# Kernel tuning notes

Measured on AMD Instinct MI355X. Metric: run time of the kernel, lower is better.

Reference implementation:

```python
import jax, jax.numpy as jnp
import numpy as np

B, S, D, V, K, H, L, U = 256, 50, 32, 10000, 16, 64, 2, 32
NORM = 0.01


def setup_inputs() -> dict:
    key = jax.random.key(0)
    ks = iter(jax.random.split(key, 64))
    r = lambda *sh: jax.random.normal(next(ks), sh, dtype=jnp.float32) * 0.05
    inp = {
        'x1': r(B, U), 'z1': r(B, S, D), 'x2': r(B, U), 'z2': r(B, S, D),
        'embd': r(V, D),
        'dec_w1': r(D, H), 'dec_b1': r(H), 'dec_w2': r(H, D), 'dec_b2': r(D),
        'i_wih': r(3 * D, D), 'i_whh': r(3 * D, D), 'i_bih': r(3 * D), 'i_bhh': r(3 * D),
        'c_wih': r(3 * D, D), 'c_whh': r(3 * D, D), 'c_bih': r(3 * D), 'c_bhh': r(3 * D),
        'im_w1': r(D, D), 'im_b1': r(D), 'im_w2': r(D, D), 'im_b2': r(D),
        'cm_w1': r(D, D), 'cm_b1': r(D), 'cm_w2': r(D, D), 'cm_b2': r(D),
        'hw1': r(L, D, K * K), 'hb1': r(L, K * K), 'hw2': r(L, D, K * K), 'hb2': r(L, K * K),
        'lin_w': r(L, U, K), 'lin_b': r(L, K), 'lout_w': r(L, K, U), 'lout_b': r(L, U),
        'sample_num': B, 'trigger_seq_length': 30,
    }
    return inp


def _gru(x, wih, whh, bih, bhh):
    # PyTorch GRU, batch_first, h0 = 0; gate order (r, z, n)
    gi = jnp.einsum('bsd,ed->bse', x, wih) + bih  # [B,S,3D]

    def step(h, gi_t):
        gh = h @ whh.T + bhh
        gir, giz, gin = jnp.split(gi_t, 3, axis=-1)
        ghr, ghz, ghn = jnp.split(gh, 3, axis=-1)
        rr = jax.nn.sigmoid(gir + ghr)
        zz = jax.nn.sigmoid(giz + ghz)
        nn = jnp.tanh(gin + rr * ghn)
        h = (1.0 - zz) * nn + zz * h
        return h, h

    h0 = jnp.zeros((x.shape[0], whh.shape[1]), x.dtype)
    _, hs = jax.lax.scan(step, h0, jnp.swapaxes(gi, 0, 1))
    return jnp.swapaxes(hs, 0, 1)  # [B,S,D]


def _forward(x1, z1, x2, z2, embd, dec_w1, dec_b1, dec_w2, dec_b2,
             i_wih, i_whh, i_bih, i_bhh, c_wih, c_whh, c_bih, c_bhh,
             im_w1, im_b1, im_w2, im_b2, cm_w1, cm_b1, cm_w2, cm_b2,
             hw1, hb1, hw2, hb2, lin_w, lin_b, lout_w, lout_b,
             sample_num, trigger_seq_length):
    # --- VQVAE.find_nearest: cdist + argmin + gather (index path has no grad) ---
    q = jax.lax.stop_gradient(z1)
    t = jax.lax.stop_gradient(embd)
    # ||q - t||^2 expanded; argmin over sqrt == argmin over squared dist
    d2 = ((q * q).sum(-1)[:, :, None]
          - 2.0 * jnp.einsum('bsd,vd->bsv', q, t)
          + (t * t).sum(-1)[None, None, :])  # [B,S,V]
    idx = jnp.argmin(d2, axis=2)  # [B,S]
    z_emb = embd[idx]  # [B,S,D], gradient flows into embd via gather

    # --- VQVAE.decode ---
    h = jax.nn.leaky_relu(z_emb @ dec_w1 + dec_b1, negative_slope=0.1)
    z_recon = h @ dec_w2 + dec_b2  # [B,S,D]

    total_loss = jnp.mean((z2 - jax.lax.stop_gradient(z_emb)) ** 2)

    # --- item branch: GRU -> pick trigger step -> MLP (tanh, linear) ---
    hs = _gru(z_recon, i_wih, i_whh, i_bih, i_bhh)
    u1 = hs[:, trigger_seq_length, :]
    z1f = jnp.tanh(u1 @ im_w1 + im_b1) @ im_w2 + im_b2  # [B,D]

    # --- category branch ---
    hs = _gru(z2, c_wih, c_whh, c_bih, c_bhh)
    u2 = hs[:, trigger_seq_length, :]
    z2f = jnp.tanh(u2 @ cm_w1 + cm_b1) @ cm_w2 + cm_b2  # [B,D]

    # --- hypernetwork layers (activations in self.modules are never applied) ---
    out = x1
    for i in range(L):
        iw = (z1f @ hw1[i] + hb1[i]).reshape(sample_num, K, K)
        cw = (z2f @ hw2[i] + hb2[i]).reshape(sample_num, K, K)
        w = jnp.clip(iw, -NORM, NORM) + cw  # [B,K,K]
        out = out @ lin_w[i] + lin_b[i]  # [B,K]
        out = jnp.einsum('bk,bkj->bj', out, w)  # bmm
        out = out @ lout_w[i] + lout_b[i]  # [B,U]
    return out, total_loss


def reference(x1, z1, x2, z2, embd, dec_w1, dec_b1, dec_w2, dec_b2,
              i_wih, i_whh, i_bih, i_bhh, c_wih, c_whh, c_bih, c_bhh,
              im_w1, im_b1, im_w2, im_b2, cm_w1, cm_b1, cm_w2, cm_b2,
              hw1, hb1, hw2, hb2, lin_w, lin_b, lout_w, lout_b,
              sample_num, trigger_seq_length):
    return _forward(x1, z1, x2, z2, embd, dec_w1, dec_b1, dec_w2, dec_b2,
                    i_wih, i_whh, i_bih, i_bhh, c_wih, c_whh, c_bih, c_bhh,
                    im_w1, im_b1, im_w2, im_b2, cm_w1, cm_b1, cm_w2, cm_b2,
                    hw1, hb1, hw2, hb2, lin_w, lin_b, lout_w, lout_b,
                    sample_num, trigger_seq_length)
```

## Files before the change

### kernel.cpp

```cpp
#include <hip/hip_runtime.h>
#include <math.h>

#define B 256
#define S 50
#define D 32
#define V 10000
#define VPAD 10240
#define KK 16
#define HH 64
#define LL 2
#define UU 32
#define TT 30
#define NROWS (B*S)
#define NORMC 0.01f
#define CH 256
#define NSLICE 10
#define SLICE_V 1024
#define VQ_RB 128

typedef __attribute__((ext_vector_type(8))) short bf16x8;
typedef __attribute__((ext_vector_type(4))) float f32x4;

__device__ __forceinline__ float sigmoidf_(float x) { return 1.0f / (1.0f + expf(-x)); }

__device__ __forceinline__ unsigned short f2bf(float x) {
    union { float f; unsigned int u; } a; a.f = x;
    unsigned int u = a.u;
    return (unsigned short)((u + 0x7FFFu + ((u >> 16) & 1u)) >> 16);
}
__device__ __forceinline__ float bf2f(unsigned short h) {
    union { unsigned int u; float f; } a; a.u = ((unsigned int)h) << 16; return a.f;
}

__device__ __forceinline__ void gld16(void* lds, const void* g) {
    __builtin_amdgcn_global_load_lds(
        (const __attribute__((address_space(1))) unsigned int*)g,
        (__attribute__((address_space(3))) unsigned int*)lds, 16, 0, 0);
}
__device__ __forceinline__ void gld4(void* lds, const void* g) {
    __builtin_amdgcn_global_load_lds(
        (const __attribute__((address_space(1))) unsigned int*)g,
        (__attribute__((address_space(3))) unsigned int*)lds, 4, 0, 0);
}

__global__ __launch_bounds__(256) void k_prep(const float* __restrict__ embd,
                                              const float* __restrict__ z1,
                                              unsigned short* __restrict__ Eh, unsigned short* __restrict__ El,
                                              unsigned short* __restrict__ Qh, unsigned short* __restrict__ Ql,
                                              float* __restrict__ tn, float* __restrict__ loss_sum,
                                              unsigned int* __restrict__ cnt) {
    int gid = blockIdx.x * 256 + threadIdx.x;
    if (gid == 0) loss_sum[0] = 0.f;
    if (gid == 1) cnt[0] = 0u;
    if (gid >= VPAD * 4 + 4 * NROWS) return;
    int isRow = (gid >= VPAD * 4);
    if (!isRow) {
        int item = gid >> 2, qd = gid & 3;
        unsigned short* dh = Eh + (size_t)item * D + qd * 8;
        unsigned short* dl = El + (size_t)item * D + qd * 8;
        if (item >= V) {
            unsigned short z[8] = {0, 0, 0, 0, 0, 0, 0, 0};
            *(uint4*)dh = *(const uint4*)z;
            *(uint4*)dl = *(const uint4*)z;
            if (qd == 0) tn[item] = INFINITY;
            return;
        }
        const float* src = embd + (size_t)item * D + qd * 8;
        float4 x0 = *(const float4*)(src);
        float4 x1 = *(const float4*)(src + 4);
        float xs[8] = {x0.x, x0.y, x0.z, x0.w, x1.x, x1.y, x1.z, x1.w};
        unsigned short hv[8], lv[8];
        float ss = 0.f;
#pragma unroll
        for (int i = 0; i < 8; i++) {
            float x = xs[i];
            ss = fmaf(x, x, ss);
            unsigned short h = f2bf(x);
            hv[i] = h;
            lv[i] = f2bf(x - bf2f(h));
        }
        *(uint4*)dh = *(const uint4*)hv;
        *(uint4*)dl = *(const uint4*)lv;
        ss += __shfl_xor(ss, 1);
        ss += __shfl_xor(ss, 2);
        if (qd == 0) tn[item] = 0.5f * ss;
    } else {
        int g = gid - VPAD * 4;
        int item = g >> 2, qd = g & 3;
        const float* src = z1 + (size_t)item * D + qd * 8;
        unsigned short* dh = Qh + (size_t)item * D + qd * 8;
        unsigned short* dl = Ql + (size_t)item * D + qd * 8;
        float4 x0 = *(const float4*)(src);
        float4 x1 = *(const float4*)(src + 4);
        float xs[8] = {x0.x, x0.y, x0.z, x0.w, x1.x, x1.y, x1.z, x1.w};
        unsigned short hv[8], lv[8];
#pragma unroll
        for (int i = 0; i < 8; i++) {
            float x = -xs[i];
            unsigned short h = f2bf(x);
            hv[i] = h;
            lv[i] = f2bf(x - bf2f(h));
        }
        *(uint4*)dh = *(const uint4*)hv;
        *(uint4*)dl = *(const uint4*)lv;
    }
}

__global__ __launch_bounds__(256, 4) void k_vq(const short* __restrict__ Qh, const short* __restrict__ Ql,
                                               const short* __restrict__ Eh, const short* __restrict__ El,
                                               const float* __restrict__ tn,
                                               float2* __restrict__ pbsv) {
    __shared__ __attribute__((aligned(16))) short EhL[CH * 32];
    __shared__ __attribute__((aligned(16))) short ElL[CH * 32];
    __shared__ float tnL[CH];
    const int tid = threadIdx.x;
    const int wave = tid >> 6, lane = tid & 63;
    const int rg = blockIdx.x / NSLICE, slice = blockIdx.x % NSLICE;
    const int row0 = rg * VQ_RB;
    const int quad = lane >> 4, c15 = lane & 15;
    const int swz = quad ^ ((c15 >> 1) & 3);
    const int ar0 = row0 + wave * 32 + c15;
    bf16x8 ah0 = *(const bf16x8*)(Qh + (size_t)ar0 * 32 + quad * 8);
    bf16x8 al0 = *(const bf16x8*)(Ql + (size_t)ar0 * 32 + quad * 8);
    bf16x8 ah1 = *(const bf16x8*)(Qh + (size_t)(ar0 + 16) * 32 + quad * 8);
    bf16x8 al1 = *(const bf16x8*)(Ql + (size_t)(ar0 + 16) * 32 + quad * 8);
    float best0[4], best1[4]; int bv0[4], bv1[4];
#pragma unroll
    for (int i = 0; i < 4; i++) {
        best0[i] = INFINITY; best1[i] = INFINITY;
        bv0[i] = 0x7fffffff; bv1[i] = 0x7fffffff;
    }
    const int vbeg = slice * SLICE_V;
    for (int c0 = 0; c0 < SLICE_V; c0 += CH) {
        __syncthreads();
        {
            const int sbS = (vbeg + c0) * 32;
#pragma unroll
            for (int i = 0; i < 4; i++) {
                int c = wave * 256 + i * 64 + lane;
                int code = c >> 2;
                int q = (c & 3) ^ ((c >> 3) & 3);
                int srcOff = sbS + code * 32 + q * 8;
                int dstOff = (wave * 256 + i * 64) * 8;
                gld16(EhL + dstOff, Eh + srcOff);
                gld16(ElL + dstOff, El + srcOff);
            }
            gld4(tnL + wave * 64, tn + vbeg + c0 + wave * 64 + lane);
        }
        __syncthreads();
#pragma unroll
        for (int t = 0; t < 16; t++) {
            const int code = t * 16 + c15;
            const int boff = code * 32 + swz * 8;
            bf16x8 bh = *(const bf16x8*)(EhL + boff);
            bf16x8 bl = *(const bf16x8*)(ElL + boff);
            const float tnv = tnL[code];
            f32x4 acc0 = {tnv, tnv, tnv, tnv};
            f32x4 acc1 = {tnv, tnv, tnv, tnv};
            acc0 = __builtin_amdgcn_mfma_f32_16x16x32_bf16(ah0, bh, acc0, 0, 0, 0);
            acc1 = __builtin_amdgcn_mfma_f32_16x16x32_bf16(ah1, bh, acc1, 0, 0, 0);
            acc0 = __builtin_amdgcn_mfma_f32_16x16x32_bf16(al0, bh, acc0, 0, 0, 0);
            acc1 = __builtin_amdgcn_mfma_f32_16x16x32_bf16(al1, bh, acc1, 0, 0, 0);
            acc0 = __builtin_amdgcn_mfma_f32_16x16x32_bf16(ah0, bl, acc0, 0, 0, 0);
            acc1 = __builtin_amdgcn_mfma_f32_16x16x32_bf16(ah1, bl, acc1, 0, 0, 0);
            const int v = vbeg + c0 + code;
#pragma unroll
            for (int i = 0; i < 4; i++) {
                float s0 = acc0[i];
                if (s0 < best0[i]) { best0[i] = s0; bv0[i] = v; }
                float s1 = acc1[i];
                if (s1 < best1[i]) { best1[i] = s1; bv1[i] = v; }
            }
        }
    }
#pragma unroll
    for (int m = 1; m <= 8; m <<= 1) {
#pragma unroll
        for (int i = 0; i < 4; i++) {
            float os = __shfl_xor(best0[i], m); int ov = __shfl_xor(bv0[i], m);
            if (os < best0[i] || (os == best0[i] && ov < bv0[i])) { best0[i] = os; bv0[i] = ov; }
            os = __shfl_xor(best1[i], m); ov = __shfl_xor(bv1[i], m);
            if (os < best1[i] || (os == best1[i] && ov < bv1[i])) { best1[i] = os; bv1[i] = ov; }
        }
    }
    if (c15 == 0) {
#pragma unroll
        for (int i = 0; i < 4; i++) {
            int r0 = row0 + wave * 32 + quad * 4 + i;
            float2 p0; p0.x = best0[i]; p0.y = __int_as_float(bv0[i]);
            pbsv[(size_t)r0 * NSLICE + slice] = p0;
            int r1 = r0 + 16;
            float2 p1; p1.x = best1[i]; p1.y = __int_as_float(bv1[i]);
            pbsv[(size_t)r1 * NSLICE + slice] = p1;
        }
    }
}

__global__ __launch_bounds__(256) void k_fused(
        const float* __restrict__ x1, const float* __restrict__ z2,
        const float* __restrict__ embd, const float2* __restrict__ pbsv,
        const float* __restrict__ dw1, const float* __restrict__ db1,
        const float* __restrict__ dw2, const float* __restrict__ db2,
        const float* __restrict__ i_wih, const float* __restrict__ i_whh,
        const float* __restrict__ i_bih, const float* __restrict__ i_bhh,
        const float* __restrict__ c_wih, const float* __restrict__ c_whh,
        const float* __restrict__ c_bih, const float* __restrict__ c_bhh,
        const float* __restrict__ im_w1, const float* __restrict__ im_b1,
        const float* __restrict__ im_w2, const float* __restrict__ im_b2,
        const float* __restrict__ cm_w1, const float* __restrict__ cm_b1,
        const float* __restrict__ cm_w2, const float* __restrict__ cm_b2,
        const float* __restrict__ hw1, const float* __restrict__ hb1,
        const float* __restrict__ hw2, const float* __restrict__ hb2,
        const float* __restrict__ lin_w, const float* __restrict__ lin_b,
        const float* __restrict__ lout_w, const float* __restrict__ lout_b,
        float* __restrict__ loss_sum, unsigned int* __restrict__ cnt,
        float* __restrict__ out) {
    __shared__ float zeL[50][33];
    __shared__ float dw1L[2048], dw2L[2048];
    __shared__ float db1L[64], db2L[32];
    __shared__ __attribute__((aligned(16))) float xsi[TT + 1][32];
    __shared__ float gii[TT + 1][96], gic[TT + 1][96];
    __shared__ float aL[TT + 1][65];
    __shared__ __attribute__((aligned(16))) float hI[2][32], hC[2][32];
    __shared__ float ghI[96], ghC[96];
    __shared__ float afL[2][32];
    __shared__ float z1fL[32], z2fL[32];
    __shared__ float wW[512];
    __shared__ float t1s[16], t2s[16], ocs[32];
    __shared__ int   vidL[50];
    __shared__ float lossRed[4];
    const int tid = threadIdx.x;
    const int b = blockIdx.x;
    const float* z2b = z2 + (size_t)b * (S * D);

    for (int p = tid; p < 2048; p += 256) { dw1L[p] = dw1[p]; dw2L[p] = dw2[p]; }
    if (tid < 64) db1L[tid] = db1[tid];
    if (tid >= 64 && tid < 96) db2L[tid - 64] = db2[tid - 64];
    if (tid < 50) {
        const float2* pp = pbsv + (size_t)(b * S + tid) * NSLICE;
        float bs = INFINITY; int bv = 0x7fffffff;
#pragma unroll
        for (int j = 0; j < NSLICE; j++) {
            float2 p = pp[j];
            int v = __float_as_int(p.y);
            if (p.x < bs) { bs = p.x; bv = v; }
        }
        vidL[tid] = bv;
    }
    __syncthreads();
    {
        const int q = tid & 7;
#pragma unroll
        for (int it = 0; it < 2; it++) {
            int s = it * 32 + (tid >> 3);
            if (s < 50) {
                float4 e4 = *(const float4*)(embd + (size_t)vidL[s] * D + q * 4);
                zeL[s][q * 4 + 0] = e4.x; zeL[s][q * 4 + 1] = e4.y;
                zeL[s][q * 4 + 2] = e4.z; zeL[s][q * 4 + 3] = e4.w;
            }
        }
    }
    __syncthreads();
    {
        const int q = tid & 7;
        float ls = 0.f;
#pragma unroll
        for (int it = 0; it < 2; it++) {
            int s = it * 32 + (tid >> 3);
            if (s < 50) {
                float4 x4 = *(const float4*)(z2b + s * D + q * 4);
                float d0 = x4.x - zeL[s][q * 4 + 0], d1 = x4.y - zeL[s][q * 4 + 1];
                float d2 = x4.z - zeL[s][q * 4 + 2], d3 = x4.w - zeL[s][q * 4 + 3];
                ls += d0 * d0 + d1 * d1 + d2 * d2 + d3 * d3;
            }
        }
#pragma unroll
        for (int off = 32; off > 0; off >>= 1) ls += __shfl_down(ls, off);
        if ((tid & 63) == 0) lossRed[tid >> 6] = ls;
        const int s = tid >> 3;
        if (s <= TT) {
#pragma unroll
            for (int j = 0; j < 8; j++) {
                int h = q * 8 + j;
                float a = db1L[h];
#pragma unroll
                for (int d = 0; d < 32; d++) a = fmaf(zeL[s][d], dw1L[d * 64 + h], a);
                aL[s][h] = (a >= 0.f) ? a : 0.1f * a;
            }
        }
    }
    __syncthreads();
    if (tid == 0) atomicAdd(loss_sum, lossRed[0] + lossRed[1] + lossRed[2] + lossRed[3]);
    {
        const int s = tid >> 3, q = tid & 7;
        if (s <= TT) {
            float zr[4];
#pragma unroll
            for (int dd = 0; dd < 4; dd++) zr[dd] = db2L[q * 4 + dd];
            for (int h = 0; h < 64; h++) {
                float av = aL[s][h];
#pragma unroll
                for (int dd = 0; dd < 4; dd++) zr[dd] = fmaf(av, dw2L[h * 32 + q * 4 + dd], zr[dd]);
            }
            float4 o4 = make_float4(zr[0], zr[1], zr[2], zr[3]);
            *(float4*)&xsi[s][q * 4] = o4;
        }
    }
    __syncthreads();
    const bool actG = (tid < 96) || (tid >= 128 && tid < 224);
    const int gru = (tid >= 128) ? 1 : 0;
    const int e = gru ? (tid - 128) : tid;
    if (actG) {
        float wihRow[32];
        const float* wg = gru ? c_wih : i_wih;
#pragma unroll
        for (int d = 0; d < 32; d++) wihRow[d] = wg[e * 32 + d];
        const float bi = (gru ? c_bih : i_bih)[e];
        float* giP = gru ? &gic[0][0] : &gii[0][0];
        for (int s = 0; s <= TT; s++) {
            float g = bi;
            if (gru) {
                const float4* xp = (const float4*)(z2b + s * D);
#pragma unroll
                for (int k = 0; k < 8; k++) {
                    float4 xv = xp[k];
                    g = fmaf(xv.x, wihRow[4 * k + 0], g);
                    g = fmaf(xv.y, wihRow[4 * k + 1], g);
                    g = fmaf(xv.z, wihRow[4 * k + 2], g);
                    g = fmaf(xv.w, wihRow[4 * k + 3], g);
                }
            } else {
                const float4* xp = (const float4*)&xsi[s][0];
#pragma unroll
                for (int k = 0; k < 8; k++) {
                    float4 xv = xp[k];
                    g = fmaf(xv.x, wihRow[4 * k + 0], g);
                    g = fmaf(xv.y, wihRow[4 * k + 1], g);
                    g = fmaf(xv.z, wihRow[4 * k + 2], g);
                    g = fmaf(xv.w, wihRow[4 * k + 3], g);
                }
            }
            giP[s * 96 + e] = g;
        }
    }
    float whhRow[32]; float bh = 0.f;
    if (actG) {
        const float* wg = gru ? c_whh : i_whh;
#pragma unroll
        for (int d = 0; d < 32; d++) whhRow[d] = wg[e * 32 + d];
        bh = (gru ? c_bhh : i_bhh)[e];
    }
    if (tid < 64) { (tid < 32 ? hI[0] : hC[0])[tid & 31] = 0.f; }
    __syncthreads();
    for (int t = 0; t <= TT; t++) {
        const int cur = t & 1;
        if (actG) {
            float g = bh;
            const float4* hp = (const float4*)(gru ? &hC[cur][0] : &hI[cur][0]);
#pragma unroll
            for (int k = 0; k < 8; k++) {
                float4 hv = hp[k];
                g = fmaf(hv.x, whhRow[4 * k + 0], g);
                g = fmaf(hv.y, whhRow[4 * k + 1], g);
                g = fmaf(hv.z, whhRow[4 * k + 2], g);
                g = fmaf(hv.w, whhRow[4 * k + 3], g);
            }
            (gru ? ghC : ghI)[e] = g;
        }
        __syncthreads();
        if (tid < 64) {
            const int g2 = tid >> 5, l = tid & 31;
            const float* giP = g2 ? &gic[t][0] : &gii[t][0];
            const float* ghP = g2 ? ghC : ghI;
            float* hP = g2 ? &hC[0][0] : &hI[0][0];
            float rr = sigmoidf_(giP[l] + ghP[l]);
            float zz = sigmoidf_(giP[l + 32] + ghP[l + 32]);
            float nn = tanhf(giP[l + 64] + rr * ghP[l + 64]);
            hP[(1 - cur) * 32 + l] = (1.f - zz) * nn + zz * hP[cur * 32 + l];
        }
        __syncthreads();
    }
    {
        const bool actM = (tid < 32) || (tid >= 128 && tid < 160);
        const int g2 = (tid >= 128) ? 1 : 0;
        const int l = tid & 31;
        if (actM) {
            const float* w1 = g2 ? cm_w1 : im_w1;
            const float* b1 = g2 ? cm_b1 : im_b1;
            const float* hP = g2 ? &hC[1][0] : &hI[1][0];
            float a = b1[l];
#pragma unroll
            for (int d = 0; d < 32; d++) a = fmaf(hP[d], w1[d * 32 + l], a);
            afL[g2][l] = tanhf(a);
        }
        __syncthreads();
        if (actM) {
            const float* w2 = g2 ? cm_w2 : im_w2;
            const float* b2 = g2 ? cm_b2 : im_b2;
            float o = b2[l];
#pragma unroll
            for (int d = 0; d < 32; d++) o = fmaf(afL[g2][d], w2[d * 32 + l], o);
            (g2 ? z2fL : z1fL)[l] = o;
        }
        if (tid < 32) ocs[tid] = x1[b * 32 + tid];
    }
    __syncthreads();
    {
        const int kk = tid;
#pragma unroll
        for (int ly = 0; ly < LL; ly++) {
            float a = hb1[ly * 256 + kk], c = hb2[ly * 256 + kk];
            const float* h1 = hw1 + ly * 8192 + kk;
            const float* h2 = hw2 + ly * 8192 + kk;
#pragma unroll
            for (int d = 0; d < 32; d++) {
                a = fmaf(z1fL[d], h1[d * 256], a);
                c = fmaf(z2fL[d], h2[d * 256], c);
            }
            a = fminf(fmaxf(a, -NORMC), NORMC);
            wW[ly * 256 + kk] = a + c;
        }
    }
    __syncthreads();
#pragma unroll
    for (int i = 0; i < LL; i++) {
        if (tid < 16) {
            float a = lin_b[i * 16 + tid];
#pragma unroll
            for (int u = 0; u < 32; u++) a = fmaf(ocs[u], lin_w[i * 512 + u * 16 + tid], a);
            t1s[tid] = a;
        }
        __syncthreads();
        if (tid < 16) {
            float a = 0.f;
#pragma unroll
            for (int k = 0; k < 16; k++) a = fmaf(t1s[k], wW[i * 256 + k * 16 + tid], a);
            t2s[tid] = a;
        }
        __syncthreads();
        if (tid < 32) {
            float a = lout_b[i * 32 + tid];
#pragma unroll
            for (int k = 0; k < 16; k++) a = fmaf(t2s[k], lout_w[i * 512 + k * 32 + tid], a);
            ocs[tid] = a;
        }
        __syncthreads();
    }
    if (tid < 32) out[(size_t)b * 32 + tid] = ocs[tid];
    if (tid == 0) {
        __threadfence();
        unsigned int old = atomicAdd(cnt, 1u);
        if (old == B - 1) {
            float tot = atomicAdd(loss_sum, 0.0f);
            out[B * UU] = tot * (1.0f / (float)(B * S * D));
        }
    }
}

extern "C" void kernel_launch(void* const* d_in, const int* in_sizes, int n_in,
                              void* d_out, int out_size, void* d_ws, size_t ws_size,
                              hipStream_t stream) {
    const float* x1     = (const float*)d_in[0];
    const float* z1     = (const float*)d_in[1];
    const float* z2     = (const float*)d_in[3];
    const float* embd   = (const float*)d_in[4];
    const float* dec_w1 = (const float*)d_in[5];
    const float* dec_b1 = (const float*)d_in[6];
    const float* dec_w2 = (const float*)d_in[7];
    const float* dec_b2 = (const float*)d_in[8];
    const float* i_wih  = (const float*)d_in[9];
    const float* i_whh  = (const float*)d_in[10];
    const float* i_bih  = (const float*)d_in[11];
    const float* i_bhh  = (const float*)d_in[12];
    const float* c_wih  = (const float*)d_in[13];
    const float* c_whh  = (const float*)d_in[14];
    const float* c_bih  = (const float*)d_in[15];
    const float* c_bhh  = (const float*)d_in[16];
    const float* im_w1  = (const float*)d_in[17];
    const float* im_b1  = (const float*)d_in[18];
    const float* im_w2  = (const float*)d_in[19];
    const float* im_b2  = (const float*)d_in[20];
    const float* cm_w1  = (const float*)d_in[21];
    const float* cm_b1  = (const float*)d_in[22];
    const float* cm_w2  = (const float*)d_in[23];
    const float* cm_b2  = (const float*)d_in[24];
    const float* hw1    = (const float*)d_in[25];
    const float* hb1    = (const float*)d_in[26];
    const float* hw2    = (const float*)d_in[27];
    const float* hb2    = (const float*)d_in[28];
    const float* lin_w  = (const float*)d_in[29];
    const float* lin_b  = (const float*)d_in[30];
    const float* lout_w = (const float*)d_in[31];
    const float* lout_b = (const float*)d_in[32];

    float* wsf      = (float*)d_ws;
    float* loss_sum = wsf;
    unsigned int* cnt = (unsigned int*)(wsf + 1);
    float* tn       = wsf + 64;
    float2* pbsv    = (float2*)(wsf + 10304);
    unsigned short* Eh = (unsigned short*)(wsf + 266304);
    unsigned short* El = (unsigned short*)(wsf + 430144);
    unsigned short* Qh = (unsigned short*)(wsf + 593984);
    unsigned short* Ql = (unsigned short*)(wsf + 798784);

    k_prep<<<(VPAD * 4 + 4 * NROWS + 255) / 256, 256, 0, stream>>>(embd, z1, Eh, El, Qh, Ql,
                                                                   tn, loss_sum, cnt);
    k_vq<<<(NROWS / VQ_RB) * NSLICE, 256, 0, stream>>>((const short*)Qh, (const short*)Ql,
                                                       (const short*)Eh, (const short*)El, tn, pbsv);
    k_fused<<<B, 256, 0, stream>>>(x1, z2, embd, pbsv,
                                   dec_w1, dec_b1, dec_w2, dec_b2,
                                   i_wih, i_whh, i_bih, i_bhh,
                                   c_wih, c_whh, c_bih, c_bhh,
                                   im_w1, im_b1, im_w2, im_b2,
                                   cm_w1, cm_b1, cm_w2, cm_b2,
                                   hw1, hb1, hw2, hb2,
                                   lin_w, lin_b, lout_w, lout_b,
                                   loss_sum, cnt, (float*)d_out);
}
```

Baseline: 196.7 us.

## Restructure VQ search per-wave without LDS and move GRU recurrence into registers

New measurement: 216.8 us. 1.1x slower.

```diff
diff --git a/kernel.cpp b/kernel.cpp
--- a/kernel.cpp
+++ b/kernel.cpp
@@ -13,10 +13,9 @@
 #define TT 30
 #define NROWS (B*S)
 #define NORMC 0.01f
-#define CH 256
-#define NSLICE 10
-#define SLICE_V 1024
-#define VQ_RB 128
+#define NSLICE 16
+#define SLICE_V 640
+#define NTILES 40
 
 typedef __attribute__((ext_vector_type(8))) short bf16x8;
 typedef __attribute__((ext_vector_type(4))) float f32x4;
@@ -32,167 +31,117 @@
     union { unsigned int u; float f; } a; a.u = ((unsigned int)h) << 16; return a.f;
 }
 
-__device__ __forceinline__ void gld16(void* lds, const void* g) {
-    __builtin_amdgcn_global_load_lds(
-        (const __attribute__((address_space(1))) unsigned int*)g,
-        (__attribute__((address_space(3))) unsigned int*)lds, 16, 0, 0);
-}
-__device__ __forceinline__ void gld4(void* lds, const void* g) {
-    __builtin_amdgcn_global_load_lds(
-        (const __attribute__((address_space(1))) unsigned int*)g,
-        (__attribute__((address_space(3))) unsigned int*)lds, 4, 0, 0);
-}
-
 __global__ __launch_bounds__(256) void k_prep(const float* __restrict__ embd,
-                                              const float* __restrict__ z1,
                                               unsigned short* __restrict__ Eh, unsigned short* __restrict__ El,
-                                              unsigned short* __restrict__ Qh, unsigned short* __restrict__ Ql,
                                               float* __restrict__ tn, float* __restrict__ loss_sum,
                                               unsigned int* __restrict__ cnt) {
     int gid = blockIdx.x * 256 + threadIdx.x;
     if (gid == 0) loss_sum[0] = 0.f;
     if (gid == 1) cnt[0] = 0u;
-    if (gid >= VPAD * 4 + 4 * NROWS) return;
-    int isRow = (gid >= VPAD * 4);
-    if (!isRow) {
-        int item = gid >> 2, qd = gid & 3;
-        unsigned short* dh = Eh + (size_t)item * D + qd * 8;
-        unsigned short* dl = El + (size_t)item * D + qd * 8;
-        if (item >= V) {
-            unsigned short z[8] = {0, 0, 0, 0, 0, 0, 0, 0};
-            *(uint4*)dh = *(const uint4*)z;
-            *(uint4*)dl = *(const uint4*)z;
-            if (qd == 0) tn[item] = INFINITY;
-            return;
-        }
-        const float* src = embd + (size_t)item * D + qd * 8;
-        float4 x0 = *(const float4*)(src);
-        float4 x1 = *(const float4*)(src + 4);
-        float xs[8] = {x0.x, x0.y, x0.z, x0.w, x1.x, x1.y, x1.z, x1.w};
-        unsigned short hv[8], lv[8];
-        float ss = 0.f;
-#pragma unroll
-        for (int i = 0; i < 8; i++) {
-            float x = xs[i];
-            ss = fmaf(x, x, ss);
-            unsigned short h = f2bf(x);
-            hv[i] = h;
-            lv[i] = f2bf(x - bf2f(h));
-        }
-        *(uint4*)dh = *(const uint4*)hv;
-        *(uint4*)dl = *(const uint4*)lv;
-        ss += __shfl_xor(ss, 1);
-        ss += __shfl_xor(ss, 2);
-        if (qd == 0) tn[item] = 0.5f * ss;
-    } else {
-        int g = gid - VPAD * 4;
-        int item = g >> 2, qd = g & 3;
-        const float* src = z1 + (size_t)item * D + qd * 8;
-        unsigned short* dh = Qh + (size_t)item * D + qd * 8;
-        unsigned short* dl = Ql + (size_t)item * D + qd * 8;
-        float4 x0 = *(const float4*)(src);
-        float4 x1 = *(const float4*)(src + 4);
-        float xs[8] = {x0.x, x0.y, x0.z, x0.w, x1.x, x1.y, x1.z, x1.w};
-        unsigned short hv[8], lv[8];
+    if (gid >= VPAD * 4) return;
+    int item = gid >> 2, qd = gid & 3;
+    unsigned short* dh = Eh + (size_t)item * D + qd * 8;
+    unsigned short* dl = El + (size_t)item * D + qd * 8;
+    if (item >= V) {
+        unsigned short z[8] = {0, 0, 0, 0, 0, 0, 0, 0};
+        *(uint4*)dh = *(const uint4*)z;
+        *(uint4*)dl = *(const uint4*)z;
+        if (qd == 0) tn[item] = INFINITY;
+        return;
+    }
+    const float* src = embd + (size_t)item * D + qd * 8;
+    float4 x0 = *(const float4*)(src);
+    float4 x1 = *(const float4*)(src + 4);
+    float xs[8] = {x0.x, x0.y, x0.z, x0.w, x1.x, x1.y, x1.z, x1.w};
+    unsigned short hv[8], lv[8];
+    float ss = 0.f;
+#pragma unroll
+    for (int i = 0; i < 8; i++) {
+        float x = xs[i];
+        ss = fmaf(x, x, ss);
+        unsigned short h = f2bf(x);
+        hv[i] = h;
+        lv[i] = f2bf(x - bf2f(h));
+    }
+    *(uint4*)dh = *(const uint4*)hv;
+    *(uint4*)dl = *(const uint4*)lv;
+    ss += __shfl_xor(ss, 1);
+    ss += __shfl_xor(ss, 2);
+    if (qd == 0) tn[item] = 0.5f * ss;
+}
+
+__global__ __launch_bounds__(256, 4) void k_vq(const float* __restrict__ z1,
+                                               const short* __restrict__ Eh, const short* __restrict__ El,
+                                               const float* __restrict__ tn,
+                                               float2* __restrict__ pbsv) {
+    const int lane = threadIdx.x & 63;
+    const int gw = blockIdx.x * 4 + (threadIdx.x >> 6);
+    const int rc = gw >> 4, slice = gw & 15;
+    const int quad = lane >> 4, c15 = lane & 15;
+    bf16x8 ah[4], al[4];
+#pragma unroll
+    for (int rt = 0; rt < 4; rt++) {
+        const float* qp = z1 + (size_t)(rc * 64 + rt * 16 + c15) * 32 + quad * 8;
+        float4 x0 = *(const float4*)qp;
+        float4 x1v = *(const float4*)(qp + 4);
+        float xs[8] = {x0.x, x0.y, x0.z, x0.w, x1v.x, x1v.y, x1v.z, x1v.w};
+        short hv[8], lv[8];
 #pragma unroll
         for (int i = 0; i < 8; i++) {
             float x = -xs[i];
             unsigned short h = f2bf(x);
-            hv[i] = h;
-            lv[i] = f2bf(x - bf2f(h));
-        }
-        *(uint4*)dh = *(const uint4*)hv;
-        *(uint4*)dl = *(const uint4*)lv;
-    }
-}
-
-__global__ __launch_bounds__(256, 4) void k_vq(const short* __restrict__ Qh, const short* __restrict__ Ql,
-                                               const short* __restrict__ Eh, const short* __restrict__ El,
-                                               const float* __restrict__ tn,
-                                               float2* __restrict__ pbsv) {
-    __shared__ __attribute__((aligned(16))) short EhL[CH * 32];
-    __shared__ __attribute__((aligned(16))) short ElL[CH * 32];
-    __shared__ float tnL[CH];
-    const int tid = threadIdx.x;
-    const int wave = tid >> 6, lane = tid & 63;
-    const int rg = blockIdx.x / NSLICE, slice = blockIdx.x % NSLICE;
-    const int row0 = rg * VQ_RB;
-    const int quad = lane >> 4, c15 = lane & 15;
-    const int swz = quad ^ ((c15 >> 1) & 3);
-    const int ar0 = row0 + wave * 32 + c15;
-    bf16x8 ah0 = *(const bf16x8*)(Qh + (size_t)ar0 * 32 + quad * 8);
-    bf16x8 al0 = *(const bf16x8*)(Ql + (size_t)ar0 * 32 + quad * 8);
-    bf16x8 ah1 = *(const bf16x8*)(Qh + (size_t)(ar0 + 16) * 32 + quad * 8);
-    bf16x8 al1 = *(const bf16x8*)(Ql + (size_t)(ar0 + 16) * 32 + quad * 8);
-    float best0[4], best1[4]; int bv0[4], bv1[4];
-#pragma unroll
-    for (int i = 0; i < 4; i++) {
-        best0[i] = INFINITY; best1[i] = INFINITY;
-        bv0[i] = 0x7fffffff; bv1[i] = 0x7fffffff;
-    }
+            hv[i] = (short)h;
+            lv[i] = (short)f2bf(x - bf2f(h));
+        }
+        ah[rt] = *(const bf16x8*)hv;
+        al[rt] = *(const bf16x8*)lv;
+    }
+    float best[4][4]; int bv[4][4];
+#pragma unroll
+    for (int rt = 0; rt < 4; rt++)
+#pragma unroll
+        for (int e = 0; e < 4; e++) { best[rt][e] = INFINITY; bv[rt][e] = 0x7fffffff; }
     const int vbeg = slice * SLICE_V;
-    for (int c0 = 0; c0 < SLICE_V; c0 += CH) {
-        __syncthreads();
-        {
-            const int sbS = (vbeg + c0) * 32;
-#pragma unroll
-            for (int i = 0; i < 4; i++) {
-                int c = wave * 256 + i * 64 + lane;
-                int code = c >> 2;
-                int q = (c & 3) ^ ((c >> 3) & 3);
-                int srcOff = sbS + code * 32 + q * 8;
-                int dstOff = (wave * 256 + i * 64) * 8;
-                gld16(EhL + dstOff, Eh + srcOff);
-                gld16(ElL + dstOff, El + srcOff);
-            }
-            gld4(tnL + wave * 64, tn + vbeg + c0 + wave * 64 + lane);
-        }
-        __syncthreads();
-#pragma unroll
-        for (int t = 0; t < 16; t++) {
-            const int code = t * 16 + c15;
-            const int boff = code * 32 + swz * 8;
-            bf16x8 bh = *(const bf16x8*)(EhL + boff);
-            bf16x8 bl = *(const bf16x8*)(ElL + boff);
-            const float tnv = tnL[code];
-            f32x4 acc0 = {tnv, tnv, tnv, tnv};
-            f32x4 acc1 = {tnv, tnv, tnv, tnv};
-            acc0 = __builtin_amdgcn_mfma_f32_16x16x32_bf16(ah0, bh, acc0, 0, 0, 0);
-            acc1 = __builtin_amdgcn_mfma_f32_16x16x32_bf16(ah1, bh, acc1, 0, 0, 0);
-            acc0 = __builtin_amdgcn_mfma_f32_16x16x32_bf16(al0, bh, acc0, 0, 0, 0);
-            acc1 = __builtin_amdgcn_mfma_f32_16x16x32_bf16(al1, bh, acc1, 0, 0, 0);
-            acc0 = __builtin_amdgcn_mfma_f32_16x16x32_bf16(ah0, bl, acc0, 0, 0, 0);
-            acc1 = __builtin_amdgcn_mfma_f32_16x16x32_bf16(ah1, bl, acc1, 0, 0, 0);
-            const int v = vbeg + c0 + code;
-#pragma unroll
-            for (int i = 0; i < 4; i++) {
-                float s0 = acc0[i];
-                if (s0 < best0[i]) { best0[i] = s0; bv0[i] = v; }
-                float s1 = acc1[i];
-                if (s1 < best1[i]) { best1[i] = s1; bv1[i] = v; }
+    for (int t = 0; t < NTILES; t++) {
+        const int code = vbeg + t * 16 + c15;
+        bf16x8 bh = *(const bf16x8*)(Eh + (size_t)code * 32 + quad * 8);
+        bf16x8 bl = *(const bf16x8*)(El + (size_t)code * 32 + quad * 8);
+        const float tnv = tn[code];
+#pragma unroll
+        for (int rt = 0; rt < 4; rt++) {
+            f32x4 acc = {tnv, tnv, tnv, tnv};
+            acc = __builtin_amdgcn_mfma_f32_16x16x32_bf16(ah[rt], bh, acc, 0, 0, 0);
+            acc = __builtin_amdgcn_mfma_f32_16x16x32_bf16(al[rt], bh, acc, 0, 0, 0);
+            acc = __builtin_amdgcn_mfma_f32_16x16x32_bf16(ah[rt], bl, acc, 0, 0, 0);
+#pragma unroll
+            for (int e = 0; e < 4; e++) {
+                float s = acc[e];
+                if (s < best[rt][e]) { best[rt][e] = s; bv[rt][e] = code; }
             }
         }
     }
 #pragma unroll
     for (int m = 1; m <= 8; m <<= 1) {
 #pragma unroll
-        for (int i = 0; i < 4; i++) {
-            float os = __shfl_xor(best0[i], m); int ov = __shfl_xor(bv0[i], m);
-            if (os < best0[i] || (os == best0[i] && ov < bv0[i])) { best0[i] = os; bv0[i] = ov; }
-            os = __shfl_xor(best1[i], m); ov = __shfl_xor(bv1[i], m);
-            if (os < best1[i] || (os == best1[i] && ov < bv1[i])) { best1[i] = os; bv1[i] = ov; }
-        }
+        for (int rt = 0; rt < 4; rt++)
+#pragma unroll
+            for (int e = 0; e < 4; e++) {
+                float os = __shfl_xor(best[rt][e], m);
+                int   ov = __shfl_xor(bv[rt][e], m);
+                if (os < best[rt][e] || (os == best[rt][e] && ov < bv[rt][e])) {
+                    best[rt][e] = os; bv[rt][e] = ov;
+                }
+            }
     }
     if (c15 == 0) {
 #pragma unroll
-        for (int i = 0; i < 4; i++) {
-            int r0 = row0 + wave * 32 + quad * 4 + i;
-            float2 p0; p0.x = best0[i]; p0.y = __int_as_float(bv0[i]);
-            pbsv[(size_t)r0 * NSLICE + slice] = p0;
-            int r1 = r0 + 16;
-            float2 p1; p1.x = best1[i]; p1.y = __int_as_float(bv1[i]);
-            pbsv[(size_t)r1 * NSLICE + slice] = p1;
-        }
+        for (int rt = 0; rt < 4; rt++)
+#pragma unroll
+            for (int e = 0; e < 4; e++) {
+                const int row = rc * 64 + rt * 16 + quad * 4 + e;
+                float2 p; p.x = best[rt][e]; p.y = __int_as_float(bv[rt][e]);
+                pbsv[(size_t)row * NSLICE + slice] = p;
+            }
     }
 }
 
@@ -221,8 +170,7 @@
     __shared__ __attribute__((aligned(16))) float xsi[TT + 1][32];
     __shared__ float gii[TT + 1][96], gic[TT + 1][96];
     __shared__ float aL[TT + 1][65];
-    __shared__ __attribute__((aligned(16))) float hI[2][32], hC[2][32];
-    __shared__ float ghI[96], ghC[96];
+    __shared__ float hI[32], hC[32];
     __shared__ float afL[2][32];
     __shared__ float z1fL[32], z2fL[32];
     __shared__ float wW[512];
@@ -282,9 +230,15 @@
 #pragma unroll
             for (int j = 0; j < 8; j++) {
                 int h = q * 8 + j;
-                float a = db1L[h];
-#pragma unroll
-                for (int d = 0; d < 32; d++) a = fmaf(zeL[s][d], dw1L[d * 64 + h], a);
+                float a0 = db1L[h], a1 = 0.f, a2 = 0.f, a3 = 0.f;
+#pragma unroll
+                for (int d = 0; d < 32; d += 4) {
+                    a0 = fmaf(zeL[s][d + 0], dw1L[(d + 0) * 64 + h], a0);
+                    a1 = fmaf(zeL[s][d + 1], dw1L[(d + 1) * 64 + h], a1);
+                    a2 = fmaf(zeL[s][d + 2], dw1L[(d + 2) * 64 + h], a2);
+                    a3 = fmaf(zeL[s][d + 3], dw1L[(d + 3) * 64 + h], a3);
+                }
+                float a = (a0 + a1) + (a2 + a3);
                 aL[s][h] = (a >= 0.f) ? a : 0.1f * a;
             }
         }
@@ -307,79 +261,70 @@
         }
     }
     __syncthreads();
-    const bool actG = (tid < 96) || (tid >= 128 && tid < 224);
-    const int gru = (tid >= 128) ? 1 : 0;
-    const int e = gru ? (tid - 128) : tid;
-    if (actG) {
-        float wihRow[32];
-        const float* wg = gru ? c_wih : i_wih;
-#pragma unroll
-        for (int d = 0; d < 32; d++) wihRow[d] = wg[e * 32 + d];
-        const float bi = (gru ? c_bih : i_bih)[e];
-        float* giP = gru ? &gic[0][0] : &gii[0][0];
-        for (int s = 0; s <= TT; s++) {
-            float g = bi;
-            if (gru) {
-                const float4* xp = (const float4*)(z2b + s * D);
+    {
+        const bool actG = (tid < 96) || (tid >= 128 && tid < 224);
+        const int gru = (tid >= 128) ? 1 : 0;
+        const int e = gru ? (tid - 128) : tid;
+        if (actG) {
+            float wihRow[32];
+            const float* wg = gru ? c_wih : i_wih;
+#pragma unroll
+            for (int d = 0; d < 32; d++) wihRow[d] = wg[e * 32 + d];
+            const float bi = (gru ? c_bih : i_bih)[e];
+            float* giP = gru ? &gic[0][0] : &gii[0][0];
+            for (int s = 0; s <= TT; s++) {
+                const float4* xp = gru ? (const float4*)(z2b + s * D)
+                                       : (const float4*)&xsi[s][0];
+                float g0 = bi, g1 = 0.f, g2a = 0.f, g3 = 0.f;
 #pragma unroll
                 for (int k = 0; k < 8; k++) {
                     float4 xv = xp[k];
-                    g = fmaf(xv.x, wihRow[4 * k + 0], g);
-                    g = fmaf(xv.y, wihRow[4 * k + 1], g);
-                    g = fmaf(xv.z, wihRow[4 * k + 2], g);
-                    g = fmaf(xv.w, wihRow[4 * k + 3], g);
+                    float* acc = (k & 3) == 0 ? &g0 : ((k & 3) == 1 ? &g1 : ((k & 3) == 2 ? &g2a : &g3));
+                    float a = *acc;
+                    a = fmaf(xv.x, wihRow[4 * k + 0], a);
+                    a = fmaf(xv.y, wihRow[4 * k + 1], a);
+                    a = fmaf(xv.z, wihRow[4 * k + 2], a);
+                    a = fmaf(xv.w, wihRow[4 * k + 3], a);
+                    *acc = a;
                 }
-            } else {
-                const float4* xp = (const float4*)&xsi[s][0];
-#pragma unroll
-                for (int k = 0; k < 8; k++) {
-                    float4 xv = xp[k];
-                    g = fmaf(xv.x, wihRow[4 * k + 0], g);
-                    g = fmaf(xv.y, wihRow[4 * k + 1], g);
-                    g = fmaf(xv.z, wihRow[4 * k + 2], g);
-                    g = fmaf(xv.w, wihRow[4 * k + 3], g);
-                }
-            }
-            giP[s * 96 + e] = g;
-        }
-    }
-    float whhRow[32]; float bh = 0.f;
-    if (actG) {
-        const float* wg = gru ? c_whh : i_whh;
-#pragma unroll
-        for (int d = 0; d < 32; d++) whhRow[d] = wg[e * 32 + d];
-        bh = (gru ? c_bhh : i_bhh)[e];
-    }
-    if (tid < 64) { (tid < 32 ? hI[0] : hC[0])[tid & 31] = 0.f; }
-    __syncthreads();
-    for (int t = 0; t <= TT; t++) {
-        const int cur = t & 1;
-        if (actG) {
-            float g = bh;
-            const float4* hp = (const float4*)(gru ? &hC[cur][0] : &hI[cur][0]);
-#pragma unroll
-            for (int k = 0; k < 8; k++) {
-                float4 hv = hp[k];
-                g = fmaf(hv.x, whhRow[4 * k + 0], g);
-                g = fmaf(hv.y, whhRow[4 * k + 1], g);
-                g = fmaf(hv.z, whhRow[4 * k + 2], g);
-                g = fmaf(hv.w, whhRow[4 * k + 3], g);
-            }
-            (gru ? ghC : ghI)[e] = g;
-        }
-        __syncthreads();
-        if (tid < 64) {
-            const int g2 = tid >> 5, l = tid & 31;
-            const float* giP = g2 ? &gic[t][0] : &gii[t][0];
-            const float* ghP = g2 ? ghC : ghI;
-            float* hP = g2 ? &hC[0][0] : &hI[0][0];
-            float rr = sigmoidf_(giP[l] + ghP[l]);
-            float zz = sigmoidf_(giP[l + 32] + ghP[l + 32]);
-            float nn = tanhf(giP[l + 64] + rr * ghP[l + 64]);
-            hP[(1 - cur) * 32 + l] = (1.f - zz) * nn + zz * hP[cur * 32 + l];
-        }
-        __syncthreads();
-    }
+                giP[s * 96 + e] = (g0 + g1) + (g2a + g3);
+            }
+        }
+    }
+    __syncthreads();
+    if (tid < 64) {
+        const int l = tid & 31;
+        const int g2 = tid >> 5;
+        const float* wg = g2 ? c_whh : i_whh;
+        float wR[32], wZ[32], wN[32];
+#pragma unroll
+        for (int d = 0; d < 32; d++) {
+            wR[d] = wg[l * 32 + d];
+            wZ[d] = wg[(l + 32) * 32 + d];
+            wN[d] = wg[(l + 64) * 32 + d];
+        }
+        const float* bg = g2 ? c_bhh : i_bhh;
+        const float bR = bg[l], bZ = bg[l + 32], bN = bg[l + 64];
+        const float* giBase = g2 ? &gic[0][0] : &gii[0][0];
+        const int src0 = g2 ? 32 : 0;
+        float hreg = 0.f;
+        for (int t = 0; t <= TT; t++) {
+            float gr = bR, gz = bZ, gn = bN;
+#pragma unroll
+            for (int d = 0; d < 32; d++) {
+                float hd = __shfl(hreg, src0 + d, 64);
+                gr = fmaf(hd, wR[d], gr);
+                gz = fmaf(hd, wZ[d], gz);
+                gn = fmaf(hd, wN[d], gn);
+            }
+            float rr = sigmoidf_(giBase[t * 96 + l] + gr);
+            float zz = sigmoidf_(giBase[t * 96 + l + 32] + gz);
+            float nn = tanhf(giBase[t * 96 + l + 64] + rr * gn);
+            hreg = (1.f - zz) * nn + zz * hreg;
+        }
+        (g2 ? hC : hI)[l] = hreg;
+    }
+    __syncthreads();
     {
         const bool actM = (tid < 32) || (tid >= 128 && tid < 160);
         const int g2 = (tid >= 128) ? 1 : 0;
@@ -387,7 +332,7 @@
         if (actM) {
             const float* w1 = g2 ? cm_w1 : im_w1;
             const float* b1 = g2 ? cm_b1 : im_b1;
-            const float* hP = g2 ? &hC[1][0] : &hI[1][0];
+            const float* hP = g2 ? hC : hI;
             float a = b1[l];
 #pragma unroll
             for (int d = 0; d < 32; d++) a = fmaf(hP[d], w1[d * 32 + l], a);
@@ -498,15 +443,12 @@
     unsigned int* cnt = (unsigned int*)(wsf + 1);
     float* tn       = wsf + 64;
     float2* pbsv    = (float2*)(wsf + 10304);
-    unsigned short* Eh = (unsigned short*)(wsf + 266304);
-    unsigned short* El = (unsigned short*)(wsf + 430144);
-    unsigned short* Qh = (unsigned short*)(wsf + 593984);
-    unsigned short* Ql = (unsigned short*)(wsf + 798784);
-
-    k_prep<<<(VPAD * 4 + 4 * NROWS + 255) / 256, 256, 0, stream>>>(embd, z1, Eh, El, Qh, Ql,
-                                                                   tn, loss_sum, cnt);
-    k_vq<<<(NROWS / VQ_RB) * NSLICE, 256, 0, stream>>>((const short*)Qh, (const short*)Ql,
-                                                       (const short*)Eh, (const short*)El, tn, pbsv);
+    unsigned short* Eh = (unsigned short*)(wsf + 419904);
+    unsigned short* El = (unsigned short*)(wsf + 583744);
+
+    k_prep<<<(VPAD * 4 + 255) / 256, 256, 0, stream>>>(embd, Eh, El, tn, loss_sum, cnt);
+    k_vq<<<(NROWS / 64) * NSLICE / 4, 256, 0, stream>>>(z1, (const short*)Eh, (const short*)El,
+                                                        tn, pbsv);
     k_fused<<<B, 256, 0, stream>>>(x1, z2, embd, pbsv,
                                    dec_w1, dec_b1, dec_w2, dec_b2,
                                    i_wih, i_whh, i_bih, i_bhh,
```
